# Performance work log

Hardware: AMD Instinct MI355X
Metric: run time of the kernel (lower is better)

Reference implementation:

```python
import jax, jax.numpy as jnp
import numpy as np

N = 8192          # batch of input points
D_IN = 4096       # input dim, power of 2
D_FEATURES = 8192 # projection dim
DEGREE = 3        # polynomial kernel degree
GAMMA = 1.0


def fwht(x):
    """Unnormalized Fast Walsh-Hadamard Transform along the last axis.
    x: (..., d) with d a power of 2. log2(d) butterfly stages."""
    orig = x.shape
    d = orig[-1]
    h = 1
    while h < d:
        y = x.reshape(orig[:-1] + (d // (2 * h), 2, h))
        a, b = y[..., 0, :], y[..., 1, :]
        x = jnp.stack([a + b, a - b], axis=-2).reshape(orig)
        h *= 2
    return x


def setup_inputs() -> dict:
    key = jax.random.key(0)
    k1, k2, k3 = jax.random.split(key, 3)
    x = jax.random.normal(k1, (N, D_IN), dtype=jnp.float32)
    # Rademacher +-1 signs, shape (degree, d_in)
    rad = jnp.where(jax.random.normal(k2, (DEGREE, D_IN)) >= 0, 1.0, -1.0).astype(jnp.float32)
    # column-sampling indices into d_in, shape (degree, d_features)
    permutations = jax.random.randint(k3, (DEGREE, D_FEATURES), 0, D_IN, dtype=jnp.int32)
    return {"x": x, "rad": rad, "permutations": permutations}


def reference(x, rad, permutations):
    # scale input, broadcast over degree, apply Rademacher signs
    z = (x * np.sqrt(GAMMA).astype(np.float32))[:, None, :] * rad  # (n, degree, d_in)
    z = fwht(z)                                                    # (n, degree, d_in)
    # gather sampled columns per degree: (n, degree, d_features)
    idx = jnp.broadcast_to(permutations[None, :, :], (z.shape[0], DEGREE, D_FEATURES))
    g = jnp.take_along_axis(z, idx, axis=2)
    # cross-degree product and normalization
    return g.prod(axis=1) / np.float32(np.sqrt(D_FEATURES))
```

## Files before the change

### kernel.cpp

```cpp
#include <hip/hip_runtime.h>
#include <hip/hip_fp16.h>

#define N_ROWS 8192
#define D_IN   4096
#define D_F    8192

typedef float f32x4 __attribute__((ext_vector_type(4)));
typedef int   i32x4 __attribute__((ext_vector_type(4)));

template<int CTRL>
__device__ __forceinline__ unsigned dppu(unsigned v) {
  int r = __builtin_amdgcn_update_dpp(0, (int)v, CTRL, 0xF, 0xF, true);
  return (unsigned)r;
}

#define DPP_QUAD_XOR1       0xB1
#define DPP_QUAD_XOR2       0x4E
#define DPP_QUAD_XOR3       0x1B
#define DPP_ROW_HALF_MIRROR 0x141
#define DPP_ROW_ROR8        0x128

__device__ __forceinline__ unsigned pkrtz(float lo, float hi) {
#if __has_builtin(__builtin_amdgcn_cvt_pkrtz)
  auto h = __builtin_amdgcn_cvt_pkrtz(lo, hi);
  return __builtin_bit_cast(unsigned, h);
#else
  __half2 h = __floats2half2_rn(lo, hi);
  return __builtin_bit_cast(unsigned, h);
#endif
}
__device__ __forceinline__ float2 upk(unsigned u) {
  return __half22float2(__builtin_bit_cast(__half2, u));
}
__device__ __forceinline__ unsigned padd(unsigned a, unsigned b) {
  return __builtin_bit_cast(unsigned,
      __hadd2(__builtin_bit_cast(__half2, a), __builtin_bit_cast(__half2, b)));
}
__device__ __forceinline__ unsigned psub(unsigned a, unsigned b) {
  return __builtin_bit_cast(unsigned,
      __hsub2(__builtin_bit_cast(__half2, a), __builtin_bit_cast(__half2, b)));
}
__device__ __forceinline__ unsigned pmul(unsigned a, unsigned b) {
  return __builtin_bit_cast(unsigned,
      __hmul2(__builtin_bit_cast(__half2, a), __builtin_bit_cast(__half2, b)));
}
__device__ __forceinline__ unsigned pfma(unsigned a, unsigned b, unsigned c) {
  return __builtin_bit_cast(unsigned,
      __hfma2(__builtin_bit_cast(__half2, a), __builtin_bit_cast(__half2, b),
              __builtin_bit_cast(__half2, c)));
}
__device__ __forceinline__ void h4p(unsigned& a, unsigned& b,
                                    unsigned& c, unsigned& d) {
  unsigned t0 = padd(a, b), t1 = psub(a, b), t2 = padd(c, d), t3 = psub(c, d);
  a = padd(t0, t2); c = psub(t0, t2);
  b = padd(t1, t3); d = psub(t1, t3);
}

__global__ __launch_bounds__(256) void srht_kernel(
    const float* __restrict__ x,
    const float* __restrict__ rad,
    const int* __restrict__ perm,
    float* __restrict__ out)
{
  __shared__ __align__(16) unsigned zp[D_IN];
  const int t    = threadIdx.x;
  const int lane = t & 63;
  const int wv   = t >> 6;
  const int n0   = blockIdx.x * 2;

  unsigned sg[6];
  #pragma unroll
  for (int s = 0; s < 6; ++s)
    sg[s] = (lane & (1 << s)) ? 0xBC00BC00u : 0x3C003C00u;

  const float S = 0.22272466f;
  unsigned xp[4][4];
  {
    const f32x4* x0 = reinterpret_cast<const f32x4*>(x) + (size_t)n0 * (D_IN / 4);
    const f32x4* x1 = x0 + (D_IN / 4);
    #pragma unroll
    for (int c = 0; c < 4; ++c) {
      f32x4 a = __builtin_nontemporal_load(x0 + c * 256 + t);
      f32x4 b = __builtin_nontemporal_load(x1 + c * 256 + t);
      xp[c][0] = pkrtz(S * a[0], S * b[0]);
      xp[c][1] = pkrtz(S * a[1], S * b[1]);
      xp[c][2] = pkrtz(S * a[2], S * b[2]);
      xp[c][3] = pkrtz(S * a[3], S * b[3]);
    }
  }

  unsigned acc[32];
  #pragma unroll
  for (int k = 0; k < 32; ++k) acc[k] = 0x34003400u;

  uint4* z4 = reinterpret_cast<uint4*>(zp);

  auto fwht_stage_trip = [&](int d, i32x4* pp) {
    unsigned v[4][4];
    const f32x4* rrow = reinterpret_cast<const f32x4*>(rad) + d * (D_IN / 4);
    #pragma unroll
    for (int c = 0; c < 4; ++c) {
      f32x4 rv = rrow[c * 256 + t];
      v[c][0] = pmul(xp[c][0], pkrtz(rv[0], rv[0]));
      v[c][1] = pmul(xp[c][1], pkrtz(rv[1], rv[1]));
      v[c][2] = pmul(xp[c][2], pkrtz(rv[2], rv[2]));
      v[c][3] = pmul(xp[c][3], pkrtz(rv[3], rv[3]));
    }
    #pragma unroll
    for (int c = 0; c < 4; ++c) h4p(v[c][0], v[c][1], v[c][2], v[c][3]);
    #pragma unroll
    for (int i = 0; i < 4; ++i) h4p(v[0][i], v[1][i], v[2][i], v[3][i]);

    #pragma unroll
    for (int c = 0; c < 4; ++c)
      #pragma unroll
      for (int i = 0; i < 4; ++i) {
        unsigned p = dppu<DPP_QUAD_XOR1>(v[c][i]);
        v[c][i] = pfma(sg[0], v[c][i], p);
      }
    #pragma unroll
    for (int c = 0; c < 4; ++c)
      #pragma unroll
      for (int i = 0; i < 4; ++i) {
        unsigned p = dppu<DPP_QUAD_XOR2>(v[c][i]);
        v[c][i] = pfma(sg[1], v[c][i], p);
      }
    #pragma unroll
    for (int c = 0; c < 4; ++c)
      #pragma unroll
      for (int i = 0; i < 4; ++i) {
        unsigned p = dppu<DPP_QUAD_XOR3>(dppu<DPP_ROW_HALF_MIRROR>(v[c][i]));
        v[c][i] = pfma(sg[2], v[c][i], p);
      }
    #pragma unroll
    for (int c = 0; c < 4; ++c)
      #pragma unroll
      for (int i = 0; i < 4; ++i) {
        unsigned p = dppu<DPP_ROW_ROR8>(v[c][i]);
        v[c][i] = pfma(sg[3], v[c][i], p);
      }
    #pragma unroll
    for (int c = 0; c < 4; ++c)
      #pragma unroll
      for (int i = 0; i < 4; ++i) {
#if __has_builtin(__builtin_amdgcn_permlane16_swap)
        auto r = __builtin_amdgcn_permlane16_swap(v[c][i], v[c][i], false, false);
        unsigned p = (lane & 16) ? (unsigned)r[0] : (unsigned)r[1];
#else
        unsigned p = (unsigned)__shfl_xor((int)v[c][i], 16, 64);
#endif
        v[c][i] = pfma(sg[4], v[c][i], p);
      }
    #pragma unroll
    for (int c = 0; c < 4; ++c)
      #pragma unroll
      for (int i = 0; i < 4; ++i) {
#if __has_builtin(__builtin_amdgcn_permlane32_swap)
        auto r = __builtin_amdgcn_permlane32_swap(v[c][i], v[c][i], false, false);
        unsigned p = (lane & 32) ? (unsigned)r[0] : (unsigned)r[1];
#else
        unsigned p = (unsigned)__shfl_xor((int)v[c][i], 32, 64);
#endif
        v[c][i] = pfma(sg[5], v[c][i], p);
      }

    const i32x4* p4 = reinterpret_cast<const i32x4*>(perm) + d * (D_F / 4);
    pp[0] = p4[0 * 256 + t];
    pp[1] = p4[1 * 256 + t];
    pp[2] = p4[2 * 256 + t];
    pp[3] = p4[3 * 256 + t];

    __syncthreads();
    #pragma unroll
    for (int c = 0; c < 4; ++c) {
      uint4 u;
      u.x = v[c][0]; u.y = v[c][1]; u.z = v[c][2]; u.w = v[c][3];
      z4[c * 256 + t] = u;
    }
    __syncthreads();

    {
      unsigned q[4][4];
      #pragma unroll
      for (int ww = 0; ww < 4; ++ww) {
        uint4 u = z4[wv * 256 + ww * 64 + lane];
        q[ww][0] = u.x; q[ww][1] = u.y; q[ww][2] = u.z; q[ww][3] = u.w;
      }
      #pragma unroll
      for (int i = 0; i < 4; ++i) h4p(q[0][i], q[1][i], q[2][i], q[3][i]);
      #pragma unroll
      for (int ww = 0; ww < 4; ++ww) {
        uint4 u;
        u.x = q[ww][0]; u.y = q[ww][1]; u.z = q[ww][2]; u.w = q[ww][3];
        z4[wv * 256 + ww * 64 + lane] = u;
      }
    }
    __syncthreads();
  };

  #pragma unroll 1
  for (int d = 0; d < 2; ++d) {
    i32x4 pp[4];
    fwht_stage_trip(d, pp);
    const i32x4* p4 = reinterpret_cast<const i32x4*>(perm) + d * (D_F / 4);
    #pragma unroll
    for (int it = 0; it < 8; ++it) {
      i32x4 p = (it < 4) ? pp[it] : p4[it * 256 + t];
      acc[it*4+0] = pmul(acc[it*4+0], zp[p[0]]);
      acc[it*4+1] = pmul(acc[it*4+1], zp[p[1]]);
      acc[it*4+2] = pmul(acc[it*4+2], zp[p[2]]);
      acc[it*4+3] = pmul(acc[it*4+3], zp[p[3]]);
    }
  }

  {
    i32x4 pp[4];
    fwht_stage_trip(2, pp);
    const i32x4* p4 = reinterpret_cast<const i32x4*>(perm) + 2 * (D_F / 4);
    f32x4* oa = reinterpret_cast<f32x4*>(out + (size_t)n0 * D_F);
    f32x4* ob = reinterpret_cast<f32x4*>(out + (size_t)(n0 + 1) * D_F);
    #pragma unroll
    for (int it = 0; it < 8; ++it) {
      i32x4 p = (it < 4) ? pp[it] : p4[it * 256 + t];
      unsigned a0 = pmul(acc[it*4+0], zp[p[0]]);
      unsigned a1 = pmul(acc[it*4+1], zp[p[1]]);
      unsigned a2 = pmul(acc[it*4+2], zp[p[2]]);
      unsigned a3 = pmul(acc[it*4+3], zp[p[3]]);
      float2 f0 = upk(a0), f1 = upk(a1), f2 = upk(a2), f3 = upk(a3);
      f32x4 va = {4.f * f0.x, 4.f * f1.x, 4.f * f2.x, 4.f * f3.x};
      f32x4 vb = {4.f * f0.y, 4.f * f1.y, 4.f * f2.y, 4.f * f3.y};
      __builtin_nontemporal_store(va, oa + it * 256 + t);
      __builtin_nontemporal_store(vb, ob + it * 256 + t);
    }
  }
}

extern "C" void kernel_launch(void* const* d_in, const int* in_sizes, int n_in,
                              void* d_out, int out_size, void* d_ws, size_t ws_size,
                              hipStream_t stream) {
  const float* x   = (const float*)d_in[0];
  const float* rad = (const float*)d_in[1];
  const int* perm  = (const int*)d_in[2];
  float* out       = (float*)d_out;
  srht_kernel<<<N_ROWS / 2, 256, 0, stream>>>(x, rad, perm, out);
}
```

Before: 83.03 us.

## Process two row-pairs per block and prefetch the next pair's input

Each block now handles two row pairs in sequence instead of one, and the grid is halved. The x loads for the next pair are issued during the last FWHT stage of the current pair so global-load latency overlaps compute and stores. This adds 32 live float registers for the raw prefetch buffer, which could lower occupancy, and the grid of 2048 blocks gives fewer waves to hide latency.

```diff
diff --git a/kernel.cpp b/kernel.cpp
--- a/kernel.cpp
+++ b/kernel.cpp
@@ -4,6 +4,7 @@
 #define N_ROWS 8192
 #define D_IN   4096
 #define D_F    8192
+#define PAIRS  2
 
 typedef float f32x4 __attribute__((ext_vector_type(4)));
 typedef int   i32x4 __attribute__((ext_vector_type(4)));
@@ -66,7 +67,7 @@
   const int t    = threadIdx.x;
   const int lane = t & 63;
   const int wv   = t >> 6;
-  const int n0   = blockIdx.x * 2;
+  const int pair0 = blockIdx.x * PAIRS;
 
   unsigned sg[6];
   #pragma unroll
@@ -75,27 +76,30 @@
 
   const float S = 0.22272466f;
   unsigned xp[4][4];
-  {
-    const f32x4* x0 = reinterpret_cast<const f32x4*>(x) + (size_t)n0 * (D_IN / 4);
+  f32x4 raw[8];
+  uint4* z4 = reinterpret_cast<uint4*>(zp);
+
+  auto load_raw = [&](int p) {
+    const f32x4* x0 = reinterpret_cast<const f32x4*>(x) +
+                      (size_t)(p * 2) * (D_IN / 4);
     const f32x4* x1 = x0 + (D_IN / 4);
     #pragma unroll
     for (int c = 0; c < 4; ++c) {
-      f32x4 a = __builtin_nontemporal_load(x0 + c * 256 + t);
-      f32x4 b = __builtin_nontemporal_load(x1 + c * 256 + t);
-      xp[c][0] = pkrtz(S * a[0], S * b[0]);
-      xp[c][1] = pkrtz(S * a[1], S * b[1]);
-      xp[c][2] = pkrtz(S * a[2], S * b[2]);
-      xp[c][3] = pkrtz(S * a[3], S * b[3]);
-    }
-  }
-
-  unsigned acc[32];
-  #pragma unroll
-  for (int k = 0; k < 32; ++k) acc[k] = 0x34003400u;
-
-  uint4* z4 = reinterpret_cast<uint4*>(zp);
-
-  auto fwht_stage_trip = [&](int d, i32x4* pp) {
+      raw[c]     = __builtin_nontemporal_load(x0 + c * 256 + t);
+      raw[4 + c] = __builtin_nontemporal_load(x1 + c * 256 + t);
+    }
+  };
+  auto pack_raw = [&]() {
+    #pragma unroll
+    for (int c = 0; c < 4; ++c) {
+      xp[c][0] = pkrtz(S * raw[c][0], S * raw[4 + c][0]);
+      xp[c][1] = pkrtz(S * raw[c][1], S * raw[4 + c][1]);
+      xp[c][2] = pkrtz(S * raw[c][2], S * raw[4 + c][2]);
+      xp[c][3] = pkrtz(S * raw[c][3], S * raw[4 + c][3]);
+    }
+  };
+
+  auto fwht_stage_trip = [&](int d, i32x4* pp, bool pf, int next_pair) {
     unsigned v[4][4];
     const f32x4* rrow = reinterpret_cast<const f32x4*>(rad) + d * (D_IN / 4);
     #pragma unroll
@@ -106,6 +110,7 @@
       v[c][2] = pmul(xp[c][2], pkrtz(rv[2], rv[2]));
       v[c][3] = pmul(xp[c][3], pkrtz(rv[3], rv[3]));
     }
+    if (pf) load_raw(next_pair);
     #pragma unroll
     for (int c = 0; c < 4; ++c) h4p(v[c][0], v[c][1], v[c][2], v[c][3]);
     #pragma unroll
@@ -198,40 +203,55 @@
     __syncthreads();
   };
 
+  load_raw(pair0);
+  pack_raw();
+
   #pragma unroll 1
-  for (int d = 0; d < 2; ++d) {
-    i32x4 pp[4];
-    fwht_stage_trip(d, pp);
-    const i32x4* p4 = reinterpret_cast<const i32x4*>(perm) + d * (D_F / 4);
-    #pragma unroll
-    for (int it = 0; it < 8; ++it) {
-      i32x4 p = (it < 4) ? pp[it] : p4[it * 256 + t];
-      acc[it*4+0] = pmul(acc[it*4+0], zp[p[0]]);
-      acc[it*4+1] = pmul(acc[it*4+1], zp[p[1]]);
-      acc[it*4+2] = pmul(acc[it*4+2], zp[p[2]]);
-      acc[it*4+3] = pmul(acc[it*4+3], zp[p[3]]);
-    }
-  }
-
-  {
-    i32x4 pp[4];
-    fwht_stage_trip(2, pp);
-    const i32x4* p4 = reinterpret_cast<const i32x4*>(perm) + 2 * (D_F / 4);
-    f32x4* oa = reinterpret_cast<f32x4*>(out + (size_t)n0 * D_F);
-    f32x4* ob = reinterpret_cast<f32x4*>(out + (size_t)(n0 + 1) * D_F);
-    #pragma unroll
-    for (int it = 0; it < 8; ++it) {
-      i32x4 p = (it < 4) ? pp[it] : p4[it * 256 + t];
-      unsigned a0 = pmul(acc[it*4+0], zp[p[0]]);
-      unsigned a1 = pmul(acc[it*4+1], zp[p[1]]);
-      unsigned a2 = pmul(acc[it*4+2], zp[p[2]]);
-      unsigned a3 = pmul(acc[it*4+3], zp[p[3]]);
-      float2 f0 = upk(a0), f1 = upk(a1), f2 = upk(a2), f3 = upk(a3);
-      f32x4 va = {4.f * f0.x, 4.f * f1.x, 4.f * f2.x, 4.f * f3.x};
-      f32x4 vb = {4.f * f0.y, 4.f * f1.y, 4.f * f2.y, 4.f * f3.y};
-      __builtin_nontemporal_store(va, oa + it * 256 + t);
-      __builtin_nontemporal_store(vb, ob + it * 256 + t);
-    }
+  for (int k = 0; k < PAIRS; ++k) {
+    const int n0 = (pair0 + k) * 2;
+    const bool pf = (k + 1 < PAIRS);
+
+    unsigned acc[32];
+    #pragma unroll
+    for (int i = 0; i < 32; ++i) acc[i] = 0x34003400u;
+
+    #pragma unroll 1
+    for (int d = 0; d < 2; ++d) {
+      i32x4 pp[4];
+      fwht_stage_trip(d, pp, false, 0);
+      const i32x4* p4 = reinterpret_cast<const i32x4*>(perm) + d * (D_F / 4);
+      #pragma unroll
+      for (int it = 0; it < 8; ++it) {
+        i32x4 p = (it < 4) ? pp[it] : p4[it * 256 + t];
+        acc[it*4+0] = pmul(acc[it*4+0], zp[p[0]]);
+        acc[it*4+1] = pmul(acc[it*4+1], zp[p[1]]);
+        acc[it*4+2] = pmul(acc[it*4+2], zp[p[2]]);
+        acc[it*4+3] = pmul(acc[it*4+3], zp[p[3]]);
+      }
+    }
+
+    {
+      i32x4 pp[4];
+      fwht_stage_trip(2, pp, pf, pair0 + k + 1);
+      const i32x4* p4 = reinterpret_cast<const i32x4*>(perm) + 2 * (D_F / 4);
+      f32x4* oa = reinterpret_cast<f32x4*>(out + (size_t)n0 * D_F);
+      f32x4* ob = reinterpret_cast<f32x4*>(out + (size_t)(n0 + 1) * D_F);
+      #pragma unroll
+      for (int it = 0; it < 8; ++it) {
+        i32x4 p = (it < 4) ? pp[it] : p4[it * 256 + t];
+        unsigned a0 = pmul(acc[it*4+0], zp[p[0]]);
+        unsigned a1 = pmul(acc[it*4+1], zp[p[1]]);
+        unsigned a2 = pmul(acc[it*4+2], zp[p[2]]);
+        unsigned a3 = pmul(acc[it*4+3], zp[p[3]]);
+        float2 f0 = upk(a0), f1 = upk(a1), f2 = upk(a2), f3 = upk(a3);
+        f32x4 va = {4.f * f0.x, 4.f * f1.x, 4.f * f2.x, 4.f * f3.x};
+        f32x4 vb = {4.f * f0.y, 4.f * f1.y, 4.f * f2.y, 4.f * f3.y};
+        __builtin_nontemporal_store(va, oa + it * 256 + t);
+        __builtin_nontemporal_store(vb, ob + it * 256 + t);
+      }
+    }
+
+    if (pf) pack_raw();
   }
 }
 
@@ -242,5 +262,5 @@
   const float* rad = (const float*)d_in[1];
   const int* perm  = (const int*)d_in[2];
   float* out       = (float*)d_out;
-  srht_kernel<<<N_ROWS / 2, 256, 0, stream>>>(x, rad, perm, out);
-}
+  srht_kernel<<<N_ROWS / 2 / PAIRS, 256, 0, stream>>>(x, rad, perm, out);
+}
```

Result: slower. 96.40 us (+16.1%).
